# Kernel optimization log

Hardware: AMD Instinct MI355X
Metric: run time of the kernel (lower is better)

Reference implementation:

```python
import jax, jax.numpy as jnp
import numpy as np

B, S, H, A, E = 64, 1024, 1024, 512, 512


def setup_inputs() -> dict:
    key = jax.random.key(0)
    ks = jax.random.split(key, 13)
    sc = 0.02
    return {
        "inputs": jax.random.normal(ks[0], (B, E), jnp.float32),
        "states": jax.random.normal(ks[1], (B, H), jnp.float32),
        "encoded": jax.random.normal(ks[2], (B, S, H), jnp.float32),
        "W_enc": jax.random.normal(ks[3], (H, A), jnp.float32) * sc,
        "b_enc": jax.random.normal(ks[4], (A,), jnp.float32) * sc,
        "W_dec": jax.random.normal(ks[5], (H, A), jnp.float32) * sc,
        "b_dec": jax.random.normal(ks[6], (A,), jnp.float32) * sc,
        "w_out": jax.random.normal(ks[7], (A,), jnp.float32) * sc,
        "b_out": jax.random.normal(ks[8], (1,), jnp.float32) * sc,
        "W_ih": jax.random.normal(ks[9], (E + H, 3 * H), jnp.float32) * sc,
        "b_ih": jax.random.normal(ks[10], (3 * H,), jnp.float32) * sc,
        "W_hh": jax.random.normal(ks[11], (H, 3 * H), jnp.float32) * sc,
        "b_hh": jax.random.normal(ks[12], (3 * H,), jnp.float32) * sc,
    }


def reference(inputs, states, encoded, W_enc, b_enc, W_dec, b_dec, w_out, b_out,
              W_ih, b_ih, W_hh, b_hh):
    # setup_memory: project encoder states once  [B,S,H] @ [H,A] -> [B,S,A]
    enc_proj = jnp.einsum('bsh,ha->bsa', encoded, W_enc) + b_enc
    # Bahdanau additive attention
    dec_proj = states @ W_dec + b_dec                       # [B,A]
    scores = jnp.einsum('bsa,a->bs', jnp.tanh(enc_proj + dec_proj[:, None, :]), w_out) + b_out[0]
    weights = jax.nn.softmax(scores, axis=1)                # [B,S]
    attention = jnp.einsum('bs,bsh->bh', weights, encoded)  # [B,H]
    x = jnp.concatenate([inputs, attention], axis=-1)       # [B,E+H]
    # GRUCell (PyTorch gate order r, z, n)
    gi = x @ W_ih + b_ih                                    # [B,3H]
    gh = states @ W_hh + b_hh                               # [B,3H]
    i_r, i_z, i_n = jnp.split(gi, 3, axis=-1)
    h_r, h_z, h_n = jnp.split(gh, 3, axis=-1)
    r = jax.nn.sigmoid(i_r + h_r)
    z = jax.nn.sigmoid(i_z + h_z)
    n = jnp.tanh(i_n + r * h_n)
    h_new = (1.0 - z) * n + z * states
    return h_new
```

## Files before the change

kernel.cpp:

```cpp
#include <hip/hip_runtime.h>
#include <hip/hip_bf16.h>


typedef __attribute__((ext_vector_type(8))) __bf16 bf16x8;
typedef __attribute__((ext_vector_type(4))) __bf16 bf16x4;
typedef __attribute__((ext_vector_type(4))) float f32x4;

__device__ __forceinline__ float fast_tanh(float x) {
  float xa = fminf(fmaxf(x, -15.f), 15.f);
  float e = __expf(2.f * xa);
  return (e - 1.f) / (e + 1.f);
}

__global__ __launch_bounds__(256) void wenc_t_kernel(const float* __restrict__ W,
                                                     __bf16* __restrict__ Wt) {
  __shared__ float tile[32][33];
  int k0 = blockIdx.x * 32, a0 = blockIdx.y * 32;
  int tid = threadIdx.x;
  int r = tid >> 3, c4 = (tid & 7) * 4;
  f32x4 v = *(const f32x4*)(W + (long)(k0 + r) * 512 + a0 + c4);
  tile[r][c4 + 0] = v.x; tile[r][c4 + 1] = v.y;
  tile[r][c4 + 2] = v.z; tile[r][c4 + 3] = v.w;
  __syncthreads();
  int a = tid >> 3, k4 = (tid & 7) * 4;
  bf16x4 o = { (__bf16)tile[k4 + 0][a], (__bf16)tile[k4 + 1][a],
               (__bf16)tile[k4 + 2][a], (__bf16)tile[k4 + 3][a] };
  *(bf16x4*)(Wt + (long)(a0 + a) * 1024 + k0 + k4) = o;
}

__global__ __launch_bounds__(256) void dec_proj_kernel(
    const float* __restrict__ states, const float* __restrict__ W_dec,
    const float* __restrict__ b_enc, const float* __restrict__ b_dec,
    float* __restrict__ addv) {
  int b = blockIdx.x, tid = threadIdx.x;
  int a = blockIdx.y * 256 + tid;
  __shared__ float sl[1024];
  for (int i = tid; i < 1024; i += 256) sl[i] = states[b * 1024 + i];
  __syncthreads();
  float c0 = 0.f, c1 = 0.f, c2 = 0.f, c3 = 0.f;
#pragma unroll 4
  for (int i = 0; i < 256; ++i) {
    c0 += sl[i]         * W_dec[(i)        * 512 + a];
    c1 += sl[i + 256]   * W_dec[(i + 256)  * 512 + a];
    c2 += sl[i + 512]   * W_dec[(i + 512)  * 512 + a];
    c3 += sl[i + 768]   * W_dec[(i + 768)  * 512 + a];
  }
  addv[b * 512 + a] = c0 + c1 + c2 + c3 + b_enc[a] + b_dec[a];
}

__global__ __launch_bounds__(512, 4) void enc_score_kernel(
    const float* __restrict__ encoded,
    const __bf16* __restrict__ Wt,
    const float* __restrict__ addv,
    const float* __restrict__ w_out,
    float* __restrict__ psc)
{
  __shared__ __attribute__((aligned(16))) char smem[34816];
  float* red = (float*)(smem + 32768);

  const int d = blockIdx.x;
  const int xcd = d & 7;
  const int slot = d >> 3;
  const int bn = slot & 3;
  const int bm = ((slot >> 2) << 3) | xcd;

  const int tid = threadIdx.x;
  const int lane = tid & 63;
  const int wid = tid >> 6;
  const int wrow = wid >> 2;
  const int wcol = wid & 3;
  const int lr = lane & 15;
  const int lkb = lane >> 4;

  const long row0 = (long)bm * 128;
  const int col0 = bn * 128;

  const int srow = tid >> 2;
  const int sk = tid & 3;
  const float* aBase = encoded + (row0 + srow) * 1024 + sk * 8;
  const __bf16* bBase = Wt + (long)(col0 + srow) * 1024 + sk * 8;
  const int wrOff = srow * 64 + ((sk ^ ((srow >> 1) & 3)) << 4);

  const int aph = ((wrow * 64 + lr) >> 1) & 3;
  const int aRd = (wrow * 64 + lr) * 64 + ((lkb ^ aph) << 4);
  const int bph = ((wcol * 32 + lr) >> 1) & 3;
  const int bRd = (wcol * 32 + lr) * 64 + ((lkb ^ bph) << 4);

  f32x4 acc[4][2];
#pragma unroll
  for (int m = 0; m < 4; ++m)
#pragma unroll
    for (int n = 0; n < 2; ++n) acc[m][n] = (f32x4){0.f, 0.f, 0.f, 0.f};

  f32x4 a0A, a1A; bf16x8 bA;
  f32x4 a0B, a1B; bf16x8 bB;

#define ISSUE(A0, A1, BV, KT) { \
    const float* _pa = aBase + (KT) * 32; \
    A0 = *(const f32x4*)_pa; \
    A1 = *(const f32x4*)(_pa + 4); \
    BV = *(const bf16x8*)(bBase + (KT) * 32); }

#define STORE(A0, A1, BV, BUFOFF) { \
    bf16x8 _wv; \
    _wv[0] = (__bf16)A0.x; _wv[1] = (__bf16)A0.y; _wv[2] = (__bf16)A0.z; _wv[3] = (__bf16)A0.w; \
    _wv[4] = (__bf16)A1.x; _wv[5] = (__bf16)A1.y; _wv[6] = (__bf16)A1.z; _wv[7] = (__bf16)A1.w; \
    *(bf16x8*)(smem + (BUFOFF) + wrOff) = _wv; \
    *(bf16x8*)(smem + 16384 + (BUFOFF) + wrOff) = BV; }

#define COMPUTE(BUFOFF) { \
    bf16x8 _af[4], _bf[2]; \
    _Pragma("unroll") for (int _m = 0; _m < 4; ++_m) \
      _af[_m] = *(const bf16x8*)(smem + (BUFOFF) + aRd + _m * 1024); \
    _Pragma("unroll") for (int _n = 0; _n < 2; ++_n) \
      _bf[_n] = *(const bf16x8*)(smem + 16384 + (BUFOFF) + bRd + _n * 1024); \
    asm volatile("s_waitcnt lgkmcnt(0)" ::: "memory"); \
    __builtin_amdgcn_sched_barrier(0); \
    __builtin_amdgcn_s_setprio(1); \
    _Pragma("unroll") for (int _m = 0; _m < 4; ++_m) \
      _Pragma("unroll") for (int _n = 0; _n < 2; ++_n) \
        acc[_m][_n] = __builtin_amdgcn_mfma_f32_16x16x32_bf16(_af[_m], _bf[_n], acc[_m][_n], 0, 0, 0); \
    __builtin_amdgcn_s_setprio(0); }

#define BAR() { \
    asm volatile("s_waitcnt lgkmcnt(0)" ::: "memory"); \
    __builtin_amdgcn_sched_barrier(0); \
    __builtin_amdgcn_s_barrier(); \
    __builtin_amdgcn_sched_barrier(0); }

  ISSUE(a0A, a1A, bA, 0);
  ISSUE(a0B, a1B, bB, 1);
  STORE(a0A, a1A, bA, 0);
  BAR();

  for (int t2 = 0; t2 < 15; ++t2) {
    ISSUE(a0A, a1A, bA, t2 * 2 + 2);
    COMPUTE(0);
    STORE(a0B, a1B, bB, 8192);
    BAR();
    ISSUE(a0B, a1B, bB, t2 * 2 + 3);
    COMPUTE(8192);
    STORE(a0A, a1A, bA, 0);
    BAR();
  }
  COMPUTE(0);
  STORE(a0B, a1B, bB, 8192);
  BAR();
  COMPUTE(8192);

#undef ISSUE
#undef STORE
#undef COMPUTE
#undef BAR

  const int b = bm >> 3;
  const float* addvb = addv + b * 512;
  float rowsum[4][4];
#pragma unroll
  for (int m = 0; m < 4; ++m)
#pragma unroll
    for (int reg = 0; reg < 4; ++reg) rowsum[m][reg] = 0.f;

#pragma unroll
  for (int m = 0; m < 4; ++m) {
#pragma unroll
    for (int n = 0; n < 2; ++n) {
      int col = col0 + wcol * 32 + n * 16 + lr;
      float av = addvb[col];
      float wo = w_out[col];
#pragma unroll
      for (int reg = 0; reg < 4; ++reg)
        rowsum[m][reg] += fast_tanh(acc[m][n][reg] + av) * wo;
    }
  }
#pragma unroll
  for (int m = 0; m < 4; ++m)
#pragma unroll
    for (int reg = 0; reg < 4; ++reg) {
      float v = rowsum[m][reg];
      v += __shfl_xor(v, 1, 64);
      v += __shfl_xor(v, 2, 64);
      v += __shfl_xor(v, 4, 64);
      v += __shfl_xor(v, 8, 64);
      rowsum[m][reg] = v;
    }
  if (lr == 0) {
#pragma unroll
    for (int m = 0; m < 4; ++m)
#pragma unroll
      for (int reg = 0; reg < 4; ++reg)
        red[(wrow * 64 + m * 16 + lkb * 4 + reg) * 4 + wcol] = rowsum[m][reg];
  }
  __syncthreads();
  if (tid < 128)
    psc[(long)bn * 65536 + row0 + tid] =
        red[tid * 4] + red[tid * 4 + 1] + red[tid * 4 + 2] + red[tid * 4 + 3];
}

__global__ __launch_bounds__(256) void softmax_kernel(const float* __restrict__ psc,
                                                      float* __restrict__ wts) {
  int b = blockIdx.x, tid = threadIdx.x;
  __shared__ float sred[8];
  float sc[4];
  float mx = -1e30f;
#pragma unroll
  for (int i = 0; i < 4; ++i) {
    long r = (long)b * 1024 + tid + i * 256;
    sc[i] = psc[r] + psc[65536 + r] + psc[2 * 65536 + r] + psc[3 * 65536 + r];
    mx = fmaxf(mx, sc[i]);
  }
  for (int off = 1; off < 64; off <<= 1) mx = fmaxf(mx, __shfl_xor(mx, off, 64));
  if ((tid & 63) == 0) sred[tid >> 6] = mx;
  __syncthreads();
  mx = fmaxf(fmaxf(sred[0], sred[1]), fmaxf(sred[2], sred[3]));
  float e[4], sum = 0.f;
#pragma unroll
  for (int i = 0; i < 4; ++i) {
    e[i] = __expf(sc[i] - mx);
    sum += e[i];
  }
  for (int off = 1; off < 64; off <<= 1) sum += __shfl_xor(sum, off, 64);
  if ((tid & 63) == 0) sred[4 + (tid >> 6)] = sum;
  __syncthreads();
  sum = sred[4] + sred[5] + sred[6] + sred[7];
  float inv = 1.f / sum;
#pragma unroll
  for (int i = 0; i < 4; ++i) wts[(long)b * 1024 + tid + i * 256] = e[i] * inv;
}

__global__ __launch_bounds__(256) void att_part_kernel(const float* __restrict__ encoded,
                                                       const float* __restrict__ wts,
                                                       float* __restrict__ attp) {
  int chunk = blockIdx.x;
  int b = blockIdx.y;
  int tid = threadIdx.x;
  f32x4 acc0 = (f32x4){0.f, 0.f, 0.f, 0.f};
  f32x4 acc1 = (f32x4){0.f, 0.f, 0.f, 0.f};
  const float* base = encoded + ((long)b * 1024 + chunk * 128) * 1024 + tid * 4;
  const float* w = wts + b * 1024 + chunk * 128;
#pragma unroll 4
  for (int s = 0; s < 128; s += 2) {
    acc0 += *(const f32x4*)(base + (long)s * 1024) * w[s];
    acc1 += *(const f32x4*)(base + (long)(s + 1) * 1024) * w[s + 1];
  }
  *(f32x4*)(attp + ((long)(b * 8 + chunk)) * 1024 + tid * 4) = acc0 + acc1;
}

__global__ __launch_bounds__(256) void xcat_kernel(const float* __restrict__ inputs,
                                                   const float* __restrict__ attp,
                                                   float* __restrict__ xcat) {
  int b = blockIdx.y;
  int k = blockIdx.x * 256 + threadIdx.x;
  float v;
  if (k < 512) {
    v = inputs[b * 512 + k];
  } else {
    int h = k - 512;
    v = 0.f;
#pragma unroll
    for (int c = 0; c < 8; ++c) v += attp[((long)(b * 8 + c)) * 1024 + h];
  }
  xcat[(long)b * 1536 + k] = v;
}

__global__ __launch_bounds__(512) void gru_gemv_kernel(
    const float* __restrict__ xcat, const float* __restrict__ states,
    const float* __restrict__ W_ih, const float* __restrict__ b_ih,
    const float* __restrict__ W_hh, const float* __restrict__ b_hh,
    float* __restrict__ gi, float* __restrict__ gh) {
  __shared__ float sx[12288];
  const int dd = blockIdx.x;
  const int xcd = dd & 7;
  const int n = dd >> 3;
  const int cgrp = xcd + 8 * (n >> 3);
  const int bg = n & 7;
  const int tid = threadIdx.x;
  const int lcol = tid & 255;
  const int bsel = (tid >> 8) * 4;

  if (cgrp < 12) {
    const int col = cgrp * 256 + lcol;
    const float* xb = xcat + (long)bg * 8 * 1536;
    for (int i = tid; i < 3072; i += 512) ((f32x4*)sx)[i] = ((const f32x4*)xb)[i];
    __syncthreads();
    float a0 = b_ih[col], a1 = a0, a2 = a0, a3 = a0;
    const float* x0 = sx + (bsel + 0) * 1536;
    const float* x1 = sx + (bsel + 1) * 1536;
    const float* x2 = sx + (bsel + 2) * 1536;
    const float* x3 = sx + (bsel + 3) * 1536;
    for (int k = 0; k < 1536; k += 4) {
      f32x4 v0 = *(const f32x4*)(x0 + k);
      f32x4 v1 = *(const f32x4*)(x1 + k);
      f32x4 v2 = *(const f32x4*)(x2 + k);
      f32x4 v3 = *(const f32x4*)(x3 + k);
#pragma unroll
      for (int j = 0; j < 4; ++j) {
        float w = W_ih[(long)(k + j) * 3072 + col];
        a0 += v0[j] * w; a1 += v1[j] * w; a2 += v2[j] * w; a3 += v3[j] * w;
      }
    }
    long o = (long)(bg * 8 + bsel) * 3072 + col;
    gi[o] = a0; gi[o + 3072] = a1; gi[o + 6144] = a2; gi[o + 9216] = a3;
  } else {
    const int col = (cgrp - 12) * 256 + lcol;
    const float* sb = states + (long)bg * 8 * 1024;
    for (int i = tid; i < 2048; i += 512) ((f32x4*)sx)[i] = ((const f32x4*)sb)[i];
    __syncthreads();
    float a0 = b_hh[col], a1 = a0, a2 = a0, a3 = a0;
    const float* x0 = sx + (bsel + 0) * 1024;
    const float* x1 = sx + (bsel + 1) * 1024;
    const float* x2 = sx + (bsel + 2) * 1024;
    const float* x3 = sx + (bsel + 3) * 1024;
    for (int k = 0; k < 1024; k += 4) {
      f32x4 v0 = *(const f32x4*)(x0 + k);
      f32x4 v1 = *(const f32x4*)(x1 + k);
      f32x4 v2 = *(const f32x4*)(x2 + k);
      f32x4 v3 = *(const f32x4*)(x3 + k);
#pragma unroll
      for (int j = 0; j < 4; ++j) {
        float w = W_hh[(long)(k + j) * 3072 + col];
        a0 += v0[j] * w; a1 += v1[j] * w; a2 += v2[j] * w; a3 += v3[j] * w;
      }
    }
    long o = (long)(bg * 8 + bsel) * 3072 + col;
    gh[o] = a0; gh[o + 3072] = a1; gh[o + 6144] = a2; gh[o + 9216] = a3;
  }
}

__global__ __launch_bounds__(256) void gate_kernel(const float* __restrict__ gi,
                                                   const float* __restrict__ gh,
                                                   const float* __restrict__ states,
                                                   float* __restrict__ out) {
  int b = blockIdx.y;
  int j = blockIdx.x * 256 + threadIdx.x;
  long o = (long)b * 3072;
  float ir = gi[o + j], hr = gh[o + j];
  float iz = gi[o + 1024 + j], hz = gh[o + 1024 + j];
  float in_ = gi[o + 2048 + j], hn = gh[o + 2048 + j];
  float r = 1.f / (1.f + __expf(-(ir + hr)));
  float z = 1.f / (1.f + __expf(-(iz + hz)));
  float n = fast_tanh(in_ + r * hn);
  out[(long)b * 1024 + j] = (1.f - z) * n + z * states[(long)b * 1024 + j];
}

extern "C" void kernel_launch(void* const* d_in, const int* in_sizes, int n_in,
                              void* d_out, int out_size, void* d_ws, size_t ws_size,
                              hipStream_t stream) {
  const float* inputs  = (const float*)d_in[0];
  const float* states  = (const float*)d_in[1];
  const float* encoded = (const float*)d_in[2];
  const float* W_enc   = (const float*)d_in[3];
  const float* b_enc   = (const float*)d_in[4];
  const float* W_dec   = (const float*)d_in[5];
  const float* b_dec   = (const float*)d_in[6];
  const float* w_out   = (const float*)d_in[7];
  const float* W_ih    = (const float*)d_in[9];
  const float* b_ih    = (const float*)d_in[10];
  const float* W_hh    = (const float*)d_in[11];
  const float* b_hh    = (const float*)d_in[12];
  float* out = (float*)d_out;
  float* ws = (float*)d_ws;

  float* addv = ws;
  float* psc  = ws + 32768;
  float* wts  = ws + 294912;
  float* attp = ws + 360448;
  float* xcat = ws + 884736;
  float* gi   = ws + 983040;
  float* gh   = ws + 1179648;
  __bf16* Wt  = (__bf16*)(ws + 1376256);

  wenc_t_kernel<<<dim3(32, 16), 256, 0, stream>>>(W_enc, Wt);

  dim3 gA(64, 2);
  dec_proj_kernel<<<gA, 256, 0, stream>>>(states, W_dec, b_enc, b_dec, addv);

  enc_score_kernel<<<2048, 512, 0, stream>>>(encoded, Wt, addv, w_out, psc);

  softmax_kernel<<<64, 256, 0, stream>>>(psc, wts);

  dim3 gD(8, 64);
  att_part_kernel<<<gD, 256, 0, stream>>>(encoded, wts, attp);

  dim3 gE(6, 64);
  xcat_kernel<<<gE, 256, 0, stream>>>(inputs, attp, xcat);

  gru_gemv_kernel<<<192, 512, 0, stream>>>(xcat, states, W_ih, b_ih, W_hh, b_hh, gi, gh);

  dim3 gG(4, 64);
  gate_kernel<<<gG, 256, 0, stream>>>(gi, gh, states, out);
}
```

Measured before the change: 328.7 us.

## Double K-tile depth in encoder-score GEMM and split attention reduction finer

The encoder-projection GEMM now stages 64-wide K tiles instead of 32, with a new XOR-swizzled shared-memory layout. This halves the number of barrier-separated pipeline steps, at the cost of doubling shared memory to 64KB, which may reduce how many blocks fit per CU. Separately, the attention weighted-sum kernel splits the sequence into 16 chunks instead of 8 and uses four accumulators. This exposes more parallelism and memory-level parallelism, while the concat kernel now sums 16 partials. Workspace offsets are moved to fit the larger partial buffer.

```diff
diff --git a/kernel.cpp b/kernel.cpp
--- a/kernel.cpp
+++ b/kernel.cpp
@@ -48,6 +48,8 @@
   addv[b * 512 + a] = c0 + c1 + c2 + c3 + b_enc[a] + b_dec[a];
 }
 
+struct Stage { f32x4 a[4]; bf16x8 b[2]; };
+
 __global__ __launch_bounds__(512, 4) void enc_score_kernel(
     const float* __restrict__ encoded,
     const __bf16* __restrict__ Wt,
@@ -55,8 +57,8 @@
     const float* __restrict__ w_out,
     float* __restrict__ psc)
 {
-  __shared__ __attribute__((aligned(16))) char smem[34816];
-  float* red = (float*)(smem + 32768);
+  __shared__ __attribute__((aligned(16))) char smem[65536];
+  float* red = (float*)smem;
 
   const int d = blockIdx.x;
   const int xcd = d & 7;
@@ -75,16 +77,20 @@
   const long row0 = (long)bm * 128;
   const int col0 = bn * 128;
 
-  const int srow = tid >> 2;
-  const int sk = tid & 3;
-  const float* aBase = encoded + (row0 + srow) * 1024 + sk * 8;
-  const __bf16* bBase = Wt + (long)(col0 + srow) * 1024 + sk * 8;
-  const int wrOff = srow * 64 + ((sk ^ ((srow >> 1) & 3)) << 4);
-
-  const int aph = ((wrow * 64 + lr) >> 1) & 3;
-  const int aRd = (wrow * 64 + lr) * 64 + ((lkb ^ aph) << 4);
-  const int bph = ((wcol * 32 + lr) >> 1) & 3;
-  const int bRd = (wcol * 32 + lr) * 64 + ((lkb ^ bph) << 4);
+  const int arow = tid >> 2, akq = tid & 3;
+  const int bcol = tid >> 2, bkq = tid & 3;
+  const float* aBase = encoded + (row0 + arow) * 1024 + akq * 16;
+  const __bf16* bBase = Wt + (long)(col0 + bcol) * 1024 + bkq * 16;
+  const int asw = (arow & 7) << 4;
+  const int aw0 = arow * 128 + ((akq * 32) ^ asw);
+  const int aw1 = arow * 128 + ((akq * 32 + 16) ^ asw);
+  const int bsw = (bcol & 7) << 4;
+  const int bw0 = bcol * 128 + ((bkq * 32) ^ bsw);
+  const int bw1 = bcol * 128 + ((bkq * 32 + 16) ^ bsw);
+
+  const int rdSw = (lkb << 4) ^ ((lr & 7) << 4);
+  const int aRow = (wrow * 64 + lr) * 128;
+  const int bRow = (wcol * 32 + lr) * 128;
 
   f32x4 acc[4][2];
 #pragma unroll
@@ -92,61 +98,72 @@
 #pragma unroll
     for (int n = 0; n < 2; ++n) acc[m][n] = (f32x4){0.f, 0.f, 0.f, 0.f};
 
-  f32x4 a0A, a1A; bf16x8 bA;
-  f32x4 a0B, a1B; bf16x8 bB;
-
-#define ISSUE(A0, A1, BV, KT) { \
-    const float* _pa = aBase + (KT) * 32; \
-    A0 = *(const f32x4*)_pa; \
-    A1 = *(const f32x4*)(_pa + 4); \
-    BV = *(const bf16x8*)(bBase + (KT) * 32); }
-
-#define STORE(A0, A1, BV, BUFOFF) { \
-    bf16x8 _wv; \
-    _wv[0] = (__bf16)A0.x; _wv[1] = (__bf16)A0.y; _wv[2] = (__bf16)A0.z; _wv[3] = (__bf16)A0.w; \
-    _wv[4] = (__bf16)A1.x; _wv[5] = (__bf16)A1.y; _wv[6] = (__bf16)A1.z; _wv[7] = (__bf16)A1.w; \
-    *(bf16x8*)(smem + (BUFOFF) + wrOff) = _wv; \
-    *(bf16x8*)(smem + 16384 + (BUFOFF) + wrOff) = BV; }
-
-#define COMPUTE(BUFOFF) { \
-    bf16x8 _af[4], _bf[2]; \
-    _Pragma("unroll") for (int _m = 0; _m < 4; ++_m) \
-      _af[_m] = *(const bf16x8*)(smem + (BUFOFF) + aRd + _m * 1024); \
-    _Pragma("unroll") for (int _n = 0; _n < 2; ++_n) \
-      _bf[_n] = *(const bf16x8*)(smem + 16384 + (BUFOFF) + bRd + _n * 1024); \
-    asm volatile("s_waitcnt lgkmcnt(0)" ::: "memory"); \
+  Stage X, Y;
+
+#define ISSUE(S, KT) do { \
+    _Pragma("unroll") for (int _j = 0; _j < 4; ++_j) \
+      S.a[_j] = *(const f32x4*)(aBase + (KT) * 64 + _j * 4); \
+    _Pragma("unroll") for (int _j = 0; _j < 2; ++_j) \
+      S.b[_j] = *(const bf16x8*)(bBase + (KT) * 64 + _j * 8); \
     __builtin_amdgcn_sched_barrier(0); \
-    __builtin_amdgcn_s_setprio(1); \
-    _Pragma("unroll") for (int _m = 0; _m < 4; ++_m) \
+  } while (0)
+
+#define STORE(S, ABUF) do { \
+    bf16x8 _w0, _w1; \
+    _Pragma("unroll") for (int _i = 0; _i < 4; ++_i) { \
+      _w0[_i] = (__bf16)S.a[0][_i]; _w0[_i + 4] = (__bf16)S.a[1][_i]; \
+      _w1[_i] = (__bf16)S.a[2][_i]; _w1[_i + 4] = (__bf16)S.a[3][_i]; } \
+    *(bf16x8*)(smem + (ABUF) + aw0) = _w0; \
+    *(bf16x8*)(smem + (ABUF) + aw1) = _w1; \
+    *(bf16x8*)(smem + 32768 + (ABUF) + bw0) = S.b[0]; \
+    *(bf16x8*)(smem + 32768 + (ABUF) + bw1) = S.b[1]; \
+    __builtin_amdgcn_sched_barrier(0); \
+  } while (0)
+
+#define COMPUTE(ABUF) do { \
+    _Pragma("unroll") for (int _ks = 0; _ks < 2; ++_ks) { \
+      bf16x8 _af[4], _bf[2]; \
+      _Pragma("unroll") for (int _m = 0; _m < 4; ++_m) \
+        _af[_m] = *(const bf16x8*)(smem + (ABUF) + aRow + _m * 2048 + (rdSw ^ (_ks << 6))); \
       _Pragma("unroll") for (int _n = 0; _n < 2; ++_n) \
-        acc[_m][_n] = __builtin_amdgcn_mfma_f32_16x16x32_bf16(_af[_m], _bf[_n], acc[_m][_n], 0, 0, 0); \
-    __builtin_amdgcn_s_setprio(0); }
-
-#define BAR() { \
+        _bf[_n] = *(const bf16x8*)(smem + 32768 + (ABUF) + bRow + _n * 2048 + (rdSw ^ (_ks << 6))); \
+      asm volatile("s_waitcnt lgkmcnt(0)" ::: "memory"); \
+      __builtin_amdgcn_sched_barrier(0); \
+      __builtin_amdgcn_s_setprio(1); \
+      _Pragma("unroll") for (int _m = 0; _m < 4; ++_m) \
+        _Pragma("unroll") for (int _n = 0; _n < 2; ++_n) \
+          acc[_m][_n] = __builtin_amdgcn_mfma_f32_16x16x32_bf16(_af[_m], _bf[_n], acc[_m][_n], 0, 0, 0); \
+      __builtin_amdgcn_s_setprio(0); \
+      __builtin_amdgcn_sched_barrier(0); \
+    } \
+  } while (0)
+
+#define BAR() do { \
     asm volatile("s_waitcnt lgkmcnt(0)" ::: "memory"); \
     __builtin_amdgcn_sched_barrier(0); \
     __builtin_amdgcn_s_barrier(); \
-    __builtin_amdgcn_sched_barrier(0); }
-
-  ISSUE(a0A, a1A, bA, 0);
-  ISSUE(a0B, a1B, bB, 1);
-  STORE(a0A, a1A, bA, 0);
+    __builtin_amdgcn_sched_barrier(0); \
+  } while (0)
+
+  ISSUE(X, 0);
+  ISSUE(Y, 1);
+  STORE(X, 0);
   BAR();
 
-  for (int t2 = 0; t2 < 15; ++t2) {
-    ISSUE(a0A, a1A, bA, t2 * 2 + 2);
+  for (int t2 = 0; t2 < 7; ++t2) {
+    ISSUE(X, 2 * t2 + 2);
     COMPUTE(0);
-    STORE(a0B, a1B, bB, 8192);
+    STORE(Y, 16384);
     BAR();
-    ISSUE(a0B, a1B, bB, t2 * 2 + 3);
-    COMPUTE(8192);
-    STORE(a0A, a1A, bA, 0);
+    ISSUE(Y, 2 * t2 + 3);
+    COMPUTE(16384);
+    STORE(X, 0);
     BAR();
   }
   COMPUTE(0);
-  STORE(a0B, a1B, bB, 8192);
+  STORE(Y, 16384);
   BAR();
-  COMPUTE(8192);
+  COMPUTE(16384);
 
 #undef ISSUE
 #undef STORE
@@ -234,16 +251,19 @@
   int chunk = blockIdx.x;
   int b = blockIdx.y;
   int tid = threadIdx.x;
-  f32x4 acc0 = (f32x4){0.f, 0.f, 0.f, 0.f};
-  f32x4 acc1 = (f32x4){0.f, 0.f, 0.f, 0.f};
-  const float* base = encoded + ((long)b * 1024 + chunk * 128) * 1024 + tid * 4;
-  const float* w = wts + b * 1024 + chunk * 128;
+  f32x4 a0 = (f32x4){0.f, 0.f, 0.f, 0.f};
+  f32x4 a1 = a0, a2 = a0, a3 = a0;
+  const float* base = encoded + ((long)b * 1024 + chunk * 64) * 1024 + tid * 4;
+  const float* w = wts + b * 1024 + chunk * 64;
 #pragma unroll 4
-  for (int s = 0; s < 128; s += 2) {
-    acc0 += *(const f32x4*)(base + (long)s * 1024) * w[s];
-    acc1 += *(const f32x4*)(base + (long)(s + 1) * 1024) * w[s + 1];
-  }
-  *(f32x4*)(attp + ((long)(b * 8 + chunk)) * 1024 + tid * 4) = acc0 + acc1;
+  for (int s = 0; s < 64; s += 4) {
+    f32x4 v0 = *(const f32x4*)(base + (long)(s + 0) * 1024);
+    f32x4 v1 = *(const f32x4*)(base + (long)(s + 1) * 1024);
+    f32x4 v2 = *(const f32x4*)(base + (long)(s + 2) * 1024);
+    f32x4 v3 = *(const f32x4*)(base + (long)(s + 3) * 1024);
+    a0 += v0 * w[s]; a1 += v1 * w[s + 1]; a2 += v2 * w[s + 2]; a3 += v3 * w[s + 3];
+  }
+  *(f32x4*)(attp + ((long)(b * 16 + chunk)) * 1024 + tid * 4) = (a0 + a1) + (a2 + a3);
 }
 
 __global__ __launch_bounds__(256) void xcat_kernel(const float* __restrict__ inputs,
@@ -258,7 +278,7 @@
     int h = k - 512;
     v = 0.f;
 #pragma unroll
-    for (int c = 0; c < 8; ++c) v += attp[((long)(b * 8 + c)) * 1024 + h];
+    for (int c = 0; c < 16; ++c) v += attp[((long)(b * 16 + c)) * 1024 + h];
   }
   xcat[(long)b * 1536 + k] = v;
 }
@@ -365,10 +385,10 @@
   float* psc  = ws + 32768;
   float* wts  = ws + 294912;
   float* attp = ws + 360448;
-  float* xcat = ws + 884736;
-  float* gi   = ws + 983040;
-  float* gh   = ws + 1179648;
-  __bf16* Wt  = (__bf16*)(ws + 1376256);
+  float* xcat = ws + 1409024;
+  float* gi   = ws + 1507328;
+  float* gh   = ws + 1703936;
+  __bf16* Wt  = (__bf16*)(ws + 1900544);
 
   wenc_t_kernel<<<dim3(32, 16), 256, 0, stream>>>(W_enc, Wt);
 
@@ -379,7 +399,7 @@
 
   softmax_kernel<<<64, 256, 0, stream>>>(psc, wts);
 
-  dim3 gD(8, 64);
+  dim3 gD(16, 64);
   att_part_kernel<<<gD, 256, 0, stream>>>(encoded, wts, attp);
 
   dim3 gE(6, 64);
```

Result: no change. 327.2 us (-0.5%).
